# Kernel optimization log

Measured on AMD Instinct MI355X. Metric: run time of the kernel, lower is better.

The kernel has to match this reference:

```python
import jax, jax.numpy as jnp
import numpy as np
from math import pi

EPS = 1e-7
GAIN = 3.5  # weight_logits_softmax_gain
MAX_LOG_VAR = 3.5


def _upper_triangular(v, T, K, D):
    # replicate tf concat([v, v[...,::-1], zeros[...,D]], axis=2) -> reshape [T,K,D,D] -> strict-upper mask
    zero_pad = jnp.zeros((T, K, D), dtype=v.dtype)
    a_flat = jnp.concatenate([v, v[..., ::-1], zero_pad], axis=2)
    a = a_flat.reshape(T, K, D, D)
    idx = jnp.arange(D)
    mask = (idx[:, None] < idx[None, :]).astype(v.dtype)
    return a * mask[None, None, :, :]


def _diag_transforms(cov_param, T, K, D):
    ut = _upper_triangular(cov_param, T, K, D)
    a = 0.5 * (jnp.swapaxes(ut, -1, -2) - ut)  # antisymmetric [T,K,D,D]
    eye = jnp.eye(D, dtype=cov_param.dtype)[None, None]
    q = jnp.matmul(eye - a, jnp.linalg.inv(eye + a))  # Cayley transform
    return q


def setup_inputs() -> dict:
    key = jax.random.key(0)
    k1, k2, k3, k4, k5 = jax.random.split(key, 5)
    B, T, K, D = 2048, 512, 8, 8
    x = jax.random.normal(k1, (B, T, D), dtype=jnp.float32)
    kernel_centers = jax.random.uniform(k2, (T, K, D), dtype=jnp.float32)
    weight_logits = jax.random.normal(k3, (T, K), dtype=jnp.float32)
    log_variance = jax.random.normal(k4, (T, K, D), dtype=jnp.float32)
    cov_param = jax.random.normal(k5, (T, K, D * (D - 1) // 2), dtype=jnp.float32)
    return {"x": x, "kernel_centers": kernel_centers, "weight_logits": weight_logits,
            "log_variance": log_variance, "cov_param": cov_param}


def reference(x, kernel_centers, weight_logits, log_variance, cov_param):
    T, K, D = kernel_centers.shape
    # subtract kernel centers: [B,T,K,D]
    xc = x[:, :, None, :] - kernel_centers[None]
    # covariance-diagonalizing rotation (Cayley transform of antisym matrix)
    q = _diag_transforms(cov_param, T, K, D)  # [T,K,D,D]
    xt = jnp.einsum('btki,tkij->btkj', xc, q)
    # per-dimension Gaussian pdf
    var = jnp.exp(jnp.clip(log_variance, -MAX_LOG_VAR, MAX_LOG_VAR))[None]  # [1,T,K,D]
    norm_coeff = 1.0 / jnp.sqrt(2.0 * pi * var)
    gaussians = norm_coeff * jnp.exp(-0.5 * xt * xt / var)  # [B,T,K,D]
    # mix: product over dims (in log space), weighted sum over kernels
    lgpe = jnp.sum(jnp.log(gaussians + EPS), axis=-1)  # [B,T,K]
    p_kernels = jnp.exp(lgpe)
    w = jax.nn.softmax(jnp.clip(weight_logits, -GAIN, GAIN), axis=-1)  # [T,K]
    p = jnp.sum(p_kernels * w[None], axis=-1)  # [B,T]
    return p
```

## Files before the change

### kernel.cpp

```cpp
#include <hip/hip_runtime.h>
#include <math.h>

#define TDIM 512
#define KDIM 8
#define DDIM 8
#define BDIM 2048

#define PSTRIDE 48
#define XSTRIDE 132

#ifndef __has_builtin
#define __has_builtin(x) 0
#endif
#if __has_builtin(__builtin_amdgcn_exp2f)
#define FAST_EXP2(x) __builtin_amdgcn_exp2f(x)
#else
#define FAST_EXP2(x) exp2f(x)
#endif

__global__ __launch_bounds__(512) void precompute_kernel(
    const float* __restrict__ centers,
    const float* __restrict__ wlogits,
    const float* __restrict__ logvar,
    const float* __restrict__ covp,
    float* __restrict__ P)
{
    const int tid = (int)blockIdx.x * 512 + (int)threadIdx.x;
    const int tk  = tid >> 3;
    const int r   = tid & 7;
    const size_t tkg = (size_t)tk;

    const float* cb = covp + tkg * 28;
    float row[8];
    #pragma unroll
    for (int j = 0; j < 8; j++) {
        const int lo = (r < j) ? r : j;
        const int hi = (r < j) ? j : r;
        const int n  = 8 * lo + hi;
        const int m  = (r == j) ? 0 : ((n < 28) ? n : 55 - n);
        const float v = cb[m];
        const float a = (r < j) ? -0.5f * v : 0.5f * v;
        row[j] = (r == j) ? 1.0f : a;
    }

    #pragma unroll
    for (int c = 0; c < 8; c++) {
        float prow[8];
        #pragma unroll
        for (int j = 0; j < 8; j++) prow[j] = __shfl(row[j], c, 8);
        const float pinv = 1.0f / prow[c];
        const float f = row[c];
        #pragma unroll
        for (int j = 0; j < 8; j++) {
            if (j == c) {
                row[j] = (r == c) ? pinv : -f * pinv;
            } else {
                const float spiv = prow[j] * pinv;
                row[j] = (r == c) ? spiv : fmaf(-f, spiv, row[j]);
            }
        }
    }
    float qr[8];
    #pragma unroll
    for (int j = 0; j < 8; j++) qr[j] = 2.0f * row[j] - (r == j ? 1.0f : 0.0f);

    const float* lvp = logvar + tkg * 8;
    float sc2[8];
    float sumlv = 0.0f;
    #pragma unroll
    for (int j = 0; j < 8; j++) {
        const float lv = fminf(fmaxf(lvp[j], -3.5f), 3.5f);
        sumlv += lv;
        sc2[j] = 0.7213475204444817f * exp2f(lv * -1.4426950408889634f);
    }
    float w[8];
    #pragma unroll
    for (int j = 0; j < 8; j++) w[j] = qr[j] * sc2[j];

    float Srow[8];
    #pragma unroll
    for (int m = 0; m < 8; m++) {
        float s = 0.0f;
        #pragma unroll
        for (int j = 0; j < 8; j++) s = fmaf(w[j], __shfl(qr[j], m, 8), s);
        Srow[m] = s;
    }

    const float* cp = centers + tkg * 8;
    float cvec[8];
    #pragma unroll
    for (int m = 0; m < 8; m++) cvec[m] = cp[m];
    float tr = 0.0f;
    #pragma unroll
    for (int m = 0; m < 8; m++) tr = fmaf(Srow[m], cvec[m], tr);
    const float lin = -2.0f * tr;
    float cpart = cp[r] * tr;
    cpart += __shfl_xor(cpart, 1, 8);
    cpart += __shfl_xor(cpart, 2, 8);
    cpart += __shfl_xor(cpart, 4, 8);

    float l = fminf(fmaxf(wlogits[tkg], -3.5f), 3.5f);
    float mx = l;
    mx = fmaxf(mx, __shfl_xor(mx, 8, 64));
    mx = fmaxf(mx, __shfl_xor(mx, 16, 64));
    mx = fmaxf(mx, __shfl_xor(mx, 32, 64));
    const float e = exp2f((l - mx) * 1.4426950408889634f);
    float ss = e;
    ss += __shfl_xor(ss, 8, 64);
    ss += __shfl_xor(ss, 16, 64);
    ss += __shfl_xor(ss, 32, 64);
    const float log2w = (l - mx) * 1.4426950408889634f - log2f(ss);
    const float slc = log2w - 10.605984517349169f - 0.7213475204444817f * sumlv;

    float* pp = P + tkg * PSTRIDE;
    const int o = 9 * r - (r * (r - 1)) / 2;
    pp[o] = lin;
    #pragma unroll
    for (int j = 0; j < 8; j++) {
        if (j >= r) pp[o + 1 + j - r] = Srow[j] * ((j == r) ? 1.0f : 2.0f);
    }
    if (r == 0) pp[44] = cpart - slc;
}

__global__ __launch_bounds__(512, 8) void pecd_main(
    const float* __restrict__ x,
    const float* __restrict__ P,
    float* __restrict__ out)
{
    __shared__ float xs[64 * XSTRIDE];

    const int tidx = (int)threadIdx.x;
    const int wv   = tidx >> 6;
    const int ln   = tidx & 63;
    const int t0   = (int)blockIdx.x * 16;
    const int b0   = (int)blockIdx.y * 64;

    #pragma unroll
    for (int it = 0; it < 4; it++) {
        const int idx = tidx + it * 512;
        const int rowi = idx >> 5;
        const int col  = idx & 31;
        const float4 v =
            *((const float4*)(x + ((size_t)(b0 + rowi) * TDIM + t0) * DDIM) + col);
        *(float4*)(xs + rowi * XSTRIDE + col * 4) = v;
    }
    __syncthreads();

    float accs[2];
    #pragma unroll
    for (int tt = 0; tt < 2; tt++) {
        const int ts = __builtin_amdgcn_readfirstlane(t0 + wv * 2 + tt);
        const float* __restrict__ pt = P + (size_t)ts * (KDIM * PSTRIDE);

        const float* xr = xs + ln * XSTRIDE + (wv * 2 + tt) * 8;
        const float4 a0 = *(const float4*)(xr);
        const float4 a1 = *(const float4*)(xr + 4);
        const float xv[8] = {a0.x, a0.y, a0.z, a0.w, a1.x, a1.y, a1.z, a1.w};

        float acc = 0.0f;
        #pragma unroll 2
        for (int k = 0; k < KDIM; k++) {
            const float* pk = pt + k * PSTRIDE;
            float e0 = pk[44], e1 = 0.0f, e2 = 0.0f, e3 = 0.0f;
            #pragma unroll
            for (int i = 0; i < 8; i++) {
                const int o = 9 * i - (i * (i - 1)) / 2;
                float inner = pk[o];
                #pragma unroll
                for (int j = i; j < 8; j++)
                    inner = fmaf(pk[o + 1 + j - i], xv[j], inner);
                if ((i & 3) == 0)      e0 = fmaf(xv[i], inner, e0);
                else if ((i & 3) == 1) e1 = fmaf(xv[i], inner, e1);
                else if ((i & 3) == 2) e2 = fmaf(xv[i], inner, e2);
                else                   e3 = fmaf(xv[i], inner, e3);
            }
            acc += FAST_EXP2(-((e0 + e1) + (e2 + e3)));
        }
        accs[tt] = acc;
    }

    __syncthreads();
    xs[ln * 18 + wv * 2 + 0] = accs[0];
    xs[ln * 18 + wv * 2 + 1] = accs[1];
    __syncthreads();
    {
        const int rowi = tidx >> 3;
        const int col  = tidx & 7;
        const float2 v = *(const float2*)&xs[rowi * 18 + col * 2];
        *(float2*)(out + (size_t)(b0 + rowi) * TDIM + t0 + col * 2) = v;
    }
}

extern "C" void kernel_launch(void* const* d_in, const int* in_sizes, int n_in,
                              void* d_out, int out_size, void* d_ws, size_t ws_size,
                              hipStream_t stream) {
    const float* x       = (const float*)d_in[0];
    const float* centers = (const float*)d_in[1];
    const float* wlogits = (const float*)d_in[2];
    const float* logvar  = (const float*)d_in[3];
    const float* covp    = (const float*)d_in[4];
    float* out = (float*)d_out;

    float* P = (float*)d_ws;

    precompute_kernel<<<dim3(TDIM * KDIM * 8 / 512), dim3(512), 0, stream>>>(
        centers, wlogits, logvar, covp, P);

    dim3 grid(TDIM / 16, BDIM / 64);
    pecd_main<<<grid, dim3(512), 0, stream>>>(x, P, out);
}
```

Before: 96.40 us.

## Fuse parameter precompute into main kernel with shared-memory params and 4-row register blocking

Merges the separate Cayley/precision precompute kernel into the main kernel: each block recomputes parameters for its 8 timesteps into LDS, so the global P workspace and second launch go away. Each thread now handles 4 batch rows for one timestep, reusing every parameter load across 4 FMA chains. The grid changes to 8 timesteps by 256 batches per block. In exchange, each parameter set is recomputed redundantly by the 8 batch-blocks, register pressure rises, and the launch bound drops to 4.

Result: faster. 93.09 us (-3.4%).

```diff
diff --git a/kernel.cpp b/kernel.cpp
--- a/kernel.cpp
+++ b/kernel.cpp
@@ -7,7 +7,7 @@
 #define BDIM 2048
 
 #define PSTRIDE 48
-#define XSTRIDE 132
+#define XSTRIDE 68
 
 #ifndef __has_builtin
 #define __has_builtin(x) 0
@@ -18,176 +18,177 @@
 #define FAST_EXP2(x) exp2f(x)
 #endif
 
-__global__ __launch_bounds__(512) void precompute_kernel(
+__global__ __launch_bounds__(512, 4) void pecd_fused(
+    const float* __restrict__ x,
     const float* __restrict__ centers,
     const float* __restrict__ wlogits,
     const float* __restrict__ logvar,
     const float* __restrict__ covp,
-    float* __restrict__ P)
-{
-    const int tid = (int)blockIdx.x * 512 + (int)threadIdx.x;
-    const int tk  = tid >> 3;
-    const int r   = tid & 7;
-    const size_t tkg = (size_t)tk;
-
-    const float* cb = covp + tkg * 28;
-    float row[8];
-    #pragma unroll
-    for (int j = 0; j < 8; j++) {
-        const int lo = (r < j) ? r : j;
-        const int hi = (r < j) ? j : r;
-        const int n  = 8 * lo + hi;
-        const int m  = (r == j) ? 0 : ((n < 28) ? n : 55 - n);
-        const float v = cb[m];
-        const float a = (r < j) ? -0.5f * v : 0.5f * v;
-        row[j] = (r == j) ? 1.0f : a;
-    }
-
-    #pragma unroll
-    for (int c = 0; c < 8; c++) {
-        float prow[8];
-        #pragma unroll
-        for (int j = 0; j < 8; j++) prow[j] = __shfl(row[j], c, 8);
-        const float pinv = 1.0f / prow[c];
-        const float f = row[c];
-        #pragma unroll
-        for (int j = 0; j < 8; j++) {
-            if (j == c) {
-                row[j] = (r == c) ? pinv : -f * pinv;
-            } else {
-                const float spiv = prow[j] * pinv;
-                row[j] = (r == c) ? spiv : fmaf(-f, spiv, row[j]);
-            }
-        }
-    }
-    float qr[8];
-    #pragma unroll
-    for (int j = 0; j < 8; j++) qr[j] = 2.0f * row[j] - (r == j ? 1.0f : 0.0f);
-
-    const float* lvp = logvar + tkg * 8;
-    float sc2[8];
-    float sumlv = 0.0f;
-    #pragma unroll
-    for (int j = 0; j < 8; j++) {
-        const float lv = fminf(fmaxf(lvp[j], -3.5f), 3.5f);
-        sumlv += lv;
-        sc2[j] = 0.7213475204444817f * exp2f(lv * -1.4426950408889634f);
-    }
-    float w[8];
-    #pragma unroll
-    for (int j = 0; j < 8; j++) w[j] = qr[j] * sc2[j];
-
-    float Srow[8];
-    #pragma unroll
-    for (int m = 0; m < 8; m++) {
-        float s = 0.0f;
-        #pragma unroll
-        for (int j = 0; j < 8; j++) s = fmaf(w[j], __shfl(qr[j], m, 8), s);
-        Srow[m] = s;
-    }
-
-    const float* cp = centers + tkg * 8;
-    float cvec[8];
-    #pragma unroll
-    for (int m = 0; m < 8; m++) cvec[m] = cp[m];
-    float tr = 0.0f;
-    #pragma unroll
-    for (int m = 0; m < 8; m++) tr = fmaf(Srow[m], cvec[m], tr);
-    const float lin = -2.0f * tr;
-    float cpart = cp[r] * tr;
-    cpart += __shfl_xor(cpart, 1, 8);
-    cpart += __shfl_xor(cpart, 2, 8);
-    cpart += __shfl_xor(cpart, 4, 8);
-
-    float l = fminf(fmaxf(wlogits[tkg], -3.5f), 3.5f);
-    float mx = l;
-    mx = fmaxf(mx, __shfl_xor(mx, 8, 64));
-    mx = fmaxf(mx, __shfl_xor(mx, 16, 64));
-    mx = fmaxf(mx, __shfl_xor(mx, 32, 64));
-    const float e = exp2f((l - mx) * 1.4426950408889634f);
-    float ss = e;
-    ss += __shfl_xor(ss, 8, 64);
-    ss += __shfl_xor(ss, 16, 64);
-    ss += __shfl_xor(ss, 32, 64);
-    const float log2w = (l - mx) * 1.4426950408889634f - log2f(ss);
-    const float slc = log2w - 10.605984517349169f - 0.7213475204444817f * sumlv;
-
-    float* pp = P + tkg * PSTRIDE;
-    const int o = 9 * r - (r * (r - 1)) / 2;
-    pp[o] = lin;
-    #pragma unroll
-    for (int j = 0; j < 8; j++) {
-        if (j >= r) pp[o + 1 + j - r] = Srow[j] * ((j == r) ? 1.0f : 2.0f);
-    }
-    if (r == 0) pp[44] = cpart - slc;
-}
-
-__global__ __launch_bounds__(512, 8) void pecd_main(
-    const float* __restrict__ x,
-    const float* __restrict__ P,
     float* __restrict__ out)
 {
+    __shared__ float prm[64 * PSTRIDE];
     __shared__ float xs[64 * XSTRIDE];
 
     const int tidx = (int)threadIdx.x;
-    const int wv   = tidx >> 6;
-    const int ln   = tidx & 63;
-    const int t0   = (int)blockIdx.x * 16;
-    const int b0   = (int)blockIdx.y * 64;
-
+    const int t0   = (int)blockIdx.x * 8;
+    const int b0   = (int)blockIdx.y * 256;
+
+    {
+        const int tk = tidx >> 3;
+        const int r  = tidx & 7;
+        const size_t tkg = (size_t)(t0 + (tk >> 3)) * 8 + (tk & 7);
+
+        const float* cb = covp + tkg * 28;
+        float row[8];
+        #pragma unroll
+        for (int j = 0; j < 8; j++) {
+            const int lo = (r < j) ? r : j;
+            const int hi = (r < j) ? j : r;
+            const int n  = 8 * lo + hi;
+            const int m  = (r == j) ? 0 : ((n < 28) ? n : 55 - n);
+            const float v = cb[m];
+            const float a = (r < j) ? -0.5f * v : 0.5f * v;
+            row[j] = (r == j) ? 1.0f : a;
+        }
+
+        #pragma unroll
+        for (int c = 0; c < 8; c++) {
+            float prow[8];
+            #pragma unroll
+            for (int j = 0; j < 8; j++) prow[j] = __shfl(row[j], c, 8);
+            const float pinv = 1.0f / prow[c];
+            const float f = row[c];
+            #pragma unroll
+            for (int j = 0; j < 8; j++) {
+                if (j == c) {
+                    row[j] = (r == c) ? pinv : -f * pinv;
+                } else {
+                    const float spiv = prow[j] * pinv;
+                    row[j] = (r == c) ? spiv : fmaf(-f, spiv, row[j]);
+                }
+            }
+        }
+        float qr[8];
+        #pragma unroll
+        for (int j = 0; j < 8; j++) qr[j] = 2.0f * row[j] - (r == j ? 1.0f : 0.0f);
+
+        const float* lvp = logvar + tkg * 8;
+        float sc2[8];
+        float sumlv = 0.0f;
+        #pragma unroll
+        for (int j = 0; j < 8; j++) {
+            const float lv = fminf(fmaxf(lvp[j], -3.5f), 3.5f);
+            sumlv += lv;
+            sc2[j] = 0.7213475204444817f * exp2f(lv * -1.4426950408889634f);
+        }
+        float w[8];
+        #pragma unroll
+        for (int j = 0; j < 8; j++) w[j] = qr[j] * sc2[j];
+
+        float Srow[8];
+        #pragma unroll
+        for (int m = 0; m < 8; m++) {
+            float s = 0.0f;
+            #pragma unroll
+            for (int j = 0; j < 8; j++) s = fmaf(w[j], __shfl(qr[j], m, 8), s);
+            Srow[m] = s;
+        }
+
+        const float* cp = centers + tkg * 8;
+        float tr = 0.0f;
+        #pragma unroll
+        for (int m = 0; m < 8; m++) tr = fmaf(Srow[m], cp[m], tr);
+        const float lin = -2.0f * tr;
+        float cpart = cp[r] * tr;
+        cpart += __shfl_xor(cpart, 1, 8);
+        cpart += __shfl_xor(cpart, 2, 8);
+        cpart += __shfl_xor(cpart, 4, 8);
+
+        float l = fminf(fmaxf(wlogits[tkg], -3.5f), 3.5f);
+        float mx = l;
+        mx = fmaxf(mx, __shfl_xor(mx, 8, 64));
+        mx = fmaxf(mx, __shfl_xor(mx, 16, 64));
+        mx = fmaxf(mx, __shfl_xor(mx, 32, 64));
+        const float e = exp2f((l - mx) * 1.4426950408889634f);
+        float ss = e;
+        ss += __shfl_xor(ss, 8, 64);
+        ss += __shfl_xor(ss, 16, 64);
+        ss += __shfl_xor(ss, 32, 64);
+        const float log2w = (l - mx) * 1.4426950408889634f - log2f(ss);
+        const float slc = log2w - 10.605984517349169f - 0.7213475204444817f * sumlv;
+
+        float* pp = prm + tk * PSTRIDE;
+        const int o = 9 * r - (r * (r - 1)) / 2;
+        pp[o] = lin;
+        #pragma unroll
+        for (int j = 0; j < 8; j++) {
+            if (j >= r) pp[o + 1 + j - r] = Srow[j] * ((j == r) ? 1.0f : 2.0f);
+        }
+        if (r == 0) pp[44] = cpart - slc;
+    }
+
+    const int wv = tidx >> 6;
+    const int ln = tidx & 63;
+
+    float xv[4][8];
     #pragma unroll
-    for (int it = 0; it < 4; it++) {
-        const int idx = tidx + it * 512;
-        const int rowi = idx >> 5;
-        const int col  = idx & 31;
-        const float4 v =
-            *((const float4*)(x + ((size_t)(b0 + rowi) * TDIM + t0) * DDIM) + col);
-        *(float4*)(xs + rowi * XSTRIDE + col * 4) = v;
-    }
-    __syncthreads();
-
-    float accs[2];
-    #pragma unroll
-    for (int tt = 0; tt < 2; tt++) {
-        const int ts = __builtin_amdgcn_readfirstlane(t0 + wv * 2 + tt);
-        const float* __restrict__ pt = P + (size_t)ts * (KDIM * PSTRIDE);
-
-        const float* xr = xs + ln * XSTRIDE + (wv * 2 + tt) * 8;
+    for (int c = 0; c < 4; c++) {
+        __syncthreads();
+        #pragma unroll
+        for (int it = 0; it < 2; it++) {
+            const int idx = tidx + it * 512;
+            const int row = idx >> 4;
+            const int col = idx & 15;
+            const float4 v =
+                *((const float4*)(x + ((size_t)(b0 + c * 64 + row) * TDIM + t0) * DDIM) + col);
+            *(float4*)(xs + row * XSTRIDE + col * 4) = v;
+        }
+        __syncthreads();
+        const float* xr = xs + ln * XSTRIDE + wv * 8;
         const float4 a0 = *(const float4*)(xr);
         const float4 a1 = *(const float4*)(xr + 4);
-        const float xv[8] = {a0.x, a0.y, a0.z, a0.w, a1.x, a1.y, a1.z, a1.w};
-
-        float acc = 0.0f;
-        #pragma unroll 2
-        for (int k = 0; k < KDIM; k++) {
-            const float* pk = pt + k * PSTRIDE;
-            float e0 = pk[44], e1 = 0.0f, e2 = 0.0f, e3 = 0.0f;
-            #pragma unroll
-            for (int i = 0; i < 8; i++) {
-                const int o = 9 * i - (i * (i - 1)) / 2;
-                float inner = pk[o];
+        xv[c][0] = a0.x; xv[c][1] = a0.y; xv[c][2] = a0.z; xv[c][3] = a0.w;
+        xv[c][4] = a1.x; xv[c][5] = a1.y; xv[c][6] = a1.z; xv[c][7] = a1.w;
+    }
+
+    float acc[4] = {0.f, 0.f, 0.f, 0.f};
+    #pragma unroll 2
+    for (int k = 0; k < KDIM; k++) {
+        const float* pk = prm + (wv * 8 + k) * PSTRIDE;
+        const float cst = pk[44];
+        float ee[4] = {cst, cst, cst, cst};
+        #pragma unroll
+        for (int i = 0; i < 8; i++) {
+            const int o = 9 * i - (i * (i - 1)) / 2;
+            const float lin = pk[o];
+            float inner[4] = {lin, lin, lin, lin};
+            #pragma unroll
+            for (int j = i; j < 8; j++) {
+                const float cf = pk[o + 1 + j - i];
                 #pragma unroll
-                for (int j = i; j < 8; j++)
-                    inner = fmaf(pk[o + 1 + j - i], xv[j], inner);
-                if ((i & 3) == 0)      e0 = fmaf(xv[i], inner, e0);
-                else if ((i & 3) == 1) e1 = fmaf(xv[i], inner, e1);
-                else if ((i & 3) == 2) e2 = fmaf(xv[i], inner, e2);
-                else                   e3 = fmaf(xv[i], inner, e3);
+                for (int c = 0; c < 4; c++) inner[c] = fmaf(cf, xv[c][j], inner[c]);
             }
-            acc += FAST_EXP2(-((e0 + e1) + (e2 + e3)));
-        }
-        accs[tt] = acc;
+            #pragma unroll
+            for (int c = 0; c < 4; c++) ee[c] = fmaf(xv[c][i], inner[c], ee[c]);
+        }
+        #pragma unroll
+        for (int c = 0; c < 4; c++) acc[c] += FAST_EXP2(-ee[c]);
     }
 
     __syncthreads();
-    xs[ln * 18 + wv * 2 + 0] = accs[0];
-    xs[ln * 18 + wv * 2 + 1] = accs[1];
+    #pragma unroll
+    for (int c = 0; c < 4; c++)
+        xs[(c * 64 + ln) * 9 + wv] = acc[c];
     __syncthreads();
     {
-        const int rowi = tidx >> 3;
-        const int col  = tidx & 7;
-        const float2 v = *(const float2*)&xs[rowi * 18 + col * 2];
-        *(float2*)(out + (size_t)(b0 + rowi) * TDIM + t0 + col * 2) = v;
+        const int row  = tidx >> 1;
+        const int part = tidx & 1;
+        float4 v;
+        v.x = xs[row * 9 + part * 4 + 0];
+        v.y = xs[row * 9 + part * 4 + 1];
+        v.z = xs[row * 9 + part * 4 + 2];
+        v.w = xs[row * 9 + part * 4 + 3];
+        *(float4*)(out + (size_t)(b0 + row) * TDIM + t0 + part * 4) = v;
     }
 }
 
@@ -200,12 +201,8 @@
     const float* logvar  = (const float*)d_in[3];
     const float* covp    = (const float*)d_in[4];
     float* out = (float*)d_out;
-
-    float* P = (float*)d_ws;
-
-    precompute_kernel<<<dim3(TDIM * KDIM * 8 / 512), dim3(512), 0, stream>>>(
-        centers, wlogits, logvar, covp, P);
-
-    dim3 grid(TDIM / 16, BDIM / 64);
-    pecd_main<<<grid, dim3(512), 0, stream>>>(x, P, out);
+    (void)d_ws; (void)ws_size;
+
+    dim3 grid(TDIM / 8, BDIM / 256);
+    pecd_fused<<<grid, dim3(512), 0, stream>>>(x, centers, wlogits, logvar, covp, out);
 }
```
